# Optimization experiments

Measured on AMD Instinct MI355X. Metric: run time of the kernel, lower is better.

## Reference

```python
import jax, jax.numpy as jnp
import numpy as np
import math

N, E, D = 50000, 800000, 128


def _linear_params(key, d_in, d_out):
    kw, kb = jax.random.split(key)
    s = 1.0 / math.sqrt(d_in)
    W = jax.random.uniform(kw, (d_out, d_in), minval=-s, maxval=s, dtype=jnp.float32)
    b = jax.random.uniform(kb, (d_out,), minval=-s, maxval=s, dtype=jnp.float32)
    return W, b


def setup_inputs() -> dict:
    key = jax.random.key(0)
    ks = jax.random.split(key, 10)
    inp = {
        "x": jax.random.normal(ks[0], (N, D), dtype=jnp.float32),
        "edge_index": jax.random.randint(ks[1], (2, E), 0, N, dtype=jnp.int32),
    }
    # BPPGraphEncoder: two attention layers, each with q/k/v linears (D->D)
    names = ["q1", "k1", "v1", "q2", "k2", "v2"]
    for i, nm in enumerate(names):
        W, b = _linear_params(ks[2 + i], D, D)
        inp[f"W{nm}"], inp[f"b{nm}"] = W, b
    # SecondaryStructureEncoder: two linears (D->D)
    inp["Ws1"], inp["bs1"] = _linear_params(ks[8], D, D)
    inp["Ws2"], inp["bs2"] = _linear_params(ks[9], D, D)
    return inp


def _attention_layer(x, row, col, Wq, bq, Wk, bk, Wv, bv):
    Q = x @ Wq.T + bq          # [N, D]
    K = x @ Wk.T + bk
    V = x @ Wv.T + bv
    # per-edge score, softmax over ALL edges (faithful to F.softmax(scores, dim=0))
    scores = jnp.sum(Q[row] * K[col], axis=-1) / math.sqrt(Q.shape[-1])  # [E]
    alpha = jax.nn.softmax(scores)                                       # [E]
    msg = alpha[:, None] * V[col]                                        # [E, D]
    return jax.ops.segment_sum(msg, row, num_segments=x.shape[0])        # [N, D]


def _ss_layer(x, row, col, W, b, deg):
    agg = jax.ops.segment_sum(x[col], row, num_segments=x.shape[0])
    return jax.nn.relu((agg / deg) @ W.T + b)


def reference(x, edge_index, Wq1, bq1, Wk1, bk1, Wv1, bv1,
              Wq2, bq2, Wk2, bk2, Wv2, bv2, Ws1, bs1, Ws2, bs2):
    row, col = edge_index[0], edge_index[1]
    # BPPGraphEncoder.forward
    h = jax.nn.elu(_attention_layer(x, row, col, Wq1, bq1, Wk1, bk1, Wv1, bv1))
    bpp_out = _attention_layer(h, row, col, Wq2, bq2, Wk2, bk2, Wv2, bv2)
    # SecondaryStructureEncoder.forward (degree-normalized message passing)
    deg = jax.ops.segment_sum(jnp.ones((row.shape[0],), jnp.float32), row,
                              num_segments=x.shape[0])
    deg = jnp.clip(deg, 1.0, None)[:, None]                              # [N, 1]
    s = _ss_layer(x, row, col, Ws1, bs1, deg)
    ss_out = _ss_layer(s, row, col, Ws2, bs2, deg)
    return jnp.concatenate([bpp_out, ss_out], axis=-1)                   # [N, 2D]
```

## Files before the change

### kernel.cpp

```cpp
#include <hip/hip_runtime.h>
#include <math.h>

#define FD 128

typedef __attribute__((ext_vector_type(8))) _Float16 half8v;
typedef __attribute__((ext_vector_type(4))) _Float16 half4v;
typedef __attribute__((ext_vector_type(4))) float float4v;
typedef __attribute__((ext_vector_type(2))) float floatx2;

static __device__ __forceinline__ void dec8(unsigned int lo, unsigned int hi, float* f){
  floatx2 a = __builtin_amdgcn_cvt_pk_f32_fp8(lo, false);
  floatx2 b = __builtin_amdgcn_cvt_pk_f32_fp8(lo, true);
  floatx2 c = __builtin_amdgcn_cvt_pk_f32_fp8(hi, false);
  floatx2 d = __builtin_amdgcn_cvt_pk_f32_fp8(hi, true);
  f[0]=a[0]; f[1]=a[1]; f[2]=b[0]; f[3]=b[1];
  f[4]=c[0]; f[5]=c[1]; f[6]=d[0]; f[7]=d[1];
}

__global__ void k_cvt_x(const float4* __restrict__ in, half4v* __restrict__ out, int n4){
  int i = blockIdx.x * 256 + threadIdx.x, st = gridDim.x * 256;
  for (; i < n4; i += st){
    float4 v = in[i];
    half4v o;
    o[0] = (_Float16)v.x; o[1] = (_Float16)v.y; o[2] = (_Float16)v.z; o[3] = (_Float16)v.w;
    out[i] = o;
  }
}

__global__ __launch_bounds__(256) void k_cvt_w(
    const float* __restrict__ w0, const float* __restrict__ w1, const float* __restrict__ w2,
    const float* __restrict__ w3, const float* __restrict__ w4, const float* __restrict__ w5,
    const float* __restrict__ w6, const float* __restrict__ w7, _Float16* __restrict__ dst){
  int i = blockIdx.x * 256 + threadIdx.x;
  if (i >= FD * FD) return;
  dst[0*FD*FD + i] = (_Float16)w0[i];
  dst[1*FD*FD + i] = (_Float16)w1[i];
  dst[2*FD*FD + i] = (_Float16)w2[i];
  dst[3*FD*FD + i] = (_Float16)w3[i];
  dst[4*FD*FD + i] = (_Float16)w4[i];
  dst[5*FD*FD + i] = (_Float16)w5[i];
  dst[6*FD*FD + i] = (_Float16)w6[i];
  dst[7*FD*FD + i] = (_Float16)w7[i];
}

__global__ void k_count_deg(const int* __restrict__ row, int E, int* __restrict__ deg){
  int i = blockIdx.x * blockDim.x + threadIdx.x;
  int stride = gridDim.x * blockDim.x;
  for (; i < E; i += stride) atomicAdd(&deg[row[i]], 1);
}

__global__ __launch_bounds__(256) void k_scan_blk(const int* __restrict__ in, int n,
    int* __restrict__ out, int* __restrict__ blksum){
  __shared__ int sm[256];
  const int tid = threadIdx.x;
  const int base = blockIdx.x * 1024;
  const int idx = base + tid * 4;
  int v0=0,v1=0,v2=0,v3=0;
  if (idx + 3 < n){ int4 t = *(const int4*)(in + idx); v0=t.x; v1=t.y; v2=t.z; v3=t.w; }
  else {
    if (idx   < n) v0 = in[idx];
    if (idx+1 < n) v1 = in[idx+1];
    if (idx+2 < n) v2 = in[idx+2];
    if (idx+3 < n) v3 = in[idx+3];
  }
  int s = v0+v1+v2+v3;
  sm[tid] = s; __syncthreads();
  for (int off = 1; off < 256; off <<= 1){
    int t = (tid >= off) ? sm[tid-off] : 0;
    __syncthreads();
    sm[tid] += t;
    __syncthreads();
  }
  int excl = sm[tid] - s;
  if (tid == 255) blksum[blockIdx.x] = sm[255];
  if (idx   < n) out[idx]   = excl;
  if (idx+1 < n) out[idx+1] = excl + v0;
  if (idx+2 < n) out[idx+2] = excl + v0 + v1;
  if (idx+3 < n) out[idx+3] = excl + v0 + v1 + v2;
}

__global__ __launch_bounds__(256) void k_scan_part(const int* __restrict__ blksum, int nblk,
    int* __restrict__ blkoff){
  __shared__ int sm[256];
  const int tid = threadIdx.x;
  int v = (tid < nblk) ? blksum[tid] : 0;
  sm[tid] = v; __syncthreads();
  for (int off = 1; off < 256; off <<= 1){
    int t = (tid >= off) ? sm[tid-off] : 0;
    __syncthreads();
    sm[tid] += t;
    __syncthreads();
  }
  if (tid < nblk) blkoff[tid] = sm[tid] - v;
}

__global__ __launch_bounds__(256) void k_scan_add(int* __restrict__ out, int n,
    const int* __restrict__ blkoff, int E){
  int i = blockIdx.x * 256 + threadIdx.x;
  if (i < n) out[i] += blkoff[i >> 10];
  if (i == 0) out[n] = E;
}

__global__ void k_fill_csr(const int* __restrict__ row, const int* __restrict__ col, int E,
                           const int* __restrict__ rowstart, int* __restrict__ cursor,
                           int* __restrict__ csrcol){
  int i = blockIdx.x * blockDim.x + threadIdx.x;
  int stride = gridDim.x * blockDim.x;
  for (; i < E; i += stride){
    int r = row[i];
    int pos = rowstart[r] + atomicAdd(&cursor[r], 1);
    csrcol[pos] = col[i];
  }
}

template<int NOUT, int ACT, int OMODE>
__global__ __launch_bounds__(256) void k_gemm_lds(const _Float16* __restrict__ X, int ldx,
    const _Float16* __restrict__ W,
    const float* __restrict__ b0, void* __restrict__ Y0,
    const float* __restrict__ b1, void* __restrict__ Y1,
    const float* __restrict__ b2, void* __restrict__ Y2,
    int ldy, int nrows)
{
  __shared__ _Float16 sW[FD * FD];
  const int tid  = threadIdx.x;
  const int wid  = tid >> 6;
  const int lane = tid & 63;
  const int l4 = lane & 15;
  const int kg = lane >> 4;
  const int r0 = blockIdx.x * 64 + wid * 16;

  int rA = r0 + l4; if (rA > nrows - 1) rA = nrows - 1;
  half8v xf[4];
  #pragma unroll
  for (int ks = 0; ks < 4; ks++)
    xf[ks] = *(const half8v*)(X + (size_t)rA * ldx + ks*32 + kg*8);

  for (int o = 0; o < NOUT; o++){
    if (o) __syncthreads();
    const _Float16* Wo = W + (size_t)o * FD * FD;
    #pragma unroll
    for (int j = 0; j < 8; j++){
      const int b = j*4096 + tid*16;
      const int row = b >> 8, cb = b & 255;
      half8v v = *(const half8v*)((const char*)Wo + b);
      *(half8v*)((char*)sW + ((row*256 + (cb ^ ((row & 7) << 4))))) = v;
    }
    __syncthreads();

    float4v acc[8];
    #pragma unroll
    for (int t = 0; t < 8; t++)
      #pragma unroll
      for (int i = 0; i < 4; i++) acc[t][i] = 0.f;

    #pragma unroll
    for (int t = 0; t < 8; t++){
      const int row = t*16 + l4;
      const int sw = (row & 7) << 4;
      #pragma unroll
      for (int ks = 0; ks < 4; ks++){
        half8v wf = *(const half8v*)((const char*)sW + (row*256 + ((ks*64 + kg*16) ^ sw)));
        acc[t] = __builtin_amdgcn_mfma_f32_16x16x32_f16(wf, xf[ks], acc[t], 0, 0, 0);
      }
    }

    const float* bo = (o == 0) ? b0 : (o == 1) ? b1 : b2;
    void* Yo = (o == 0) ? Y0 : (o == 1) ? Y1 : Y2;
    const int r = r0 + l4;
    if (r < nrows){
      #pragma unroll
      for (int t = 0; t < 8; t++){
        const int c = t*16 + kg*4;
        const float4 bb = *(const float4*)(bo + c);
        float v0 = acc[t][0] + bb.x, v1 = acc[t][1] + bb.y;
        float v2 = acc[t][2] + bb.z, v3 = acc[t][3] + bb.w;
        if (ACT){ v0=fmaxf(v0,0.f); v1=fmaxf(v1,0.f); v2=fmaxf(v2,0.f); v3=fmaxf(v3,0.f); }
        if (OMODE == 1 && o == 0){
          *(float4*)((float*)Yo + (size_t)r * ldy + c) = make_float4(v0, v1, v2, v3);
        } else if (OMODE == 2 && o > 0){
          unsigned int w01 = (unsigned int)__builtin_amdgcn_cvt_pk_fp8_f32(v0, v1, 0, false);
          unsigned int w   = (unsigned int)__builtin_amdgcn_cvt_pk_fp8_f32(v2, v3, (int)w01, true);
          *(unsigned int*)((unsigned char*)Yo + (size_t)r * FD + c) = w;
        } else {
          half4v hv;
          hv[0]=(_Float16)v0; hv[1]=(_Float16)v1; hv[2]=(_Float16)v2; hv[3]=(_Float16)v3;
          *(half4v*)((_Float16*)Yo + (size_t)r * ldy + c) = hv;
        }
      }
    }
  }
}

#define SC 0.08838834764831845f

#define RED16(d) \
  d += __shfl_xor(d, 1); d += __shfl_xor(d, 2); d += __shfl_xor(d, 4); d += __shfl_xor(d, 8);

__global__ __launch_bounds__(256) void k_passA(const _Float16* __restrict__ Qh,
    const unsigned char* __restrict__ K8, const _Float16* __restrict__ Xh,
    const int* __restrict__ rowstart, const int* __restrict__ csrcol,
    float* __restrict__ scores, _Float16* __restrict__ SMh, int ldsm, int nnodes)
{
  const int tid = threadIdx.x;
  const int n = blockIdx.x * 16 + (tid >> 4);
  if (n >= nnodes) return;
  const int l4 = tid & 15;
  const half8v qv = *(const half8v*)(Qh + (size_t)n * FD + 8*l4);
  float qf[8];
  #pragma unroll
  for (int i = 0; i < 8; i++) qf[i] = (float)qv[i];
  float sx[8];
  #pragma unroll
  for (int i = 0; i < 8; i++) sx[i] = 0.f;
  const int p0 = rowstart[n], p1 = rowstart[n+1];
  const int last = p1 - 1;
  for (int p = p0; p < p1; p += 4){
    int cc[4]; float mk[4];
    #pragma unroll
    for (int j = 0; j < 4; j++){
      const int idx = p + j;
      cc[j] = csrcol[idx < p1 ? idx : last];
      mk[j] = idx < p1 ? 1.f : 0.f;
    }
    uint2 ku[4]; half8v xv[4];
    #pragma unroll
    for (int j = 0; j < 4; j++){
      ku[j] = *(const uint2*)(K8 + (size_t)cc[j]*FD + 8*l4);
      xv[j] = *(const half8v*)(Xh + (size_t)cc[j]*FD + 8*l4);
    }
    float d[4];
    #pragma unroll
    for (int j = 0; j < 4; j++){
      float kf[8];
      dec8(ku[j].x, ku[j].y, kf);
      float t = 0.f;
      #pragma unroll
      for (int i = 0; i < 8; i++) t += qf[i] * kf[i];
      d[j] = t;
      #pragma unroll
      for (int i = 0; i < 8; i++) sx[i] += mk[j] * (float)xv[j][i];
    }
    #pragma unroll
    for (int j = 0; j < 4; j++){ RED16(d[j]) }
    const float sv = (l4==0) ? d[0] : (l4==1) ? d[1] : (l4==2) ? d[2] : d[3];
    if (l4 < 4 && p + l4 < p1) scores[p + l4] = sv * SC;
  }
  int dg = p1 - p0; if (dg < 1) dg = 1;
  const float inv = 1.f / (float)dg;
  half8v o;
  #pragma unroll
  for (int i = 0; i < 8; i++) o[i] = (_Float16)(sx[i]*inv);
  *(half8v*)(SMh + (size_t)n * ldsm + 8*l4) = o;
}

__global__ __launch_bounds__(256) void k_scores2(const _Float16* __restrict__ Qh,
    const unsigned char* __restrict__ K8,
    const int* __restrict__ rowstart, const int* __restrict__ csrcol,
    float* __restrict__ scores, int nnodes)
{
  const int tid = threadIdx.x;
  const int n = blockIdx.x * 16 + (tid >> 4);
  if (n >= nnodes) return;
  const int l4 = tid & 15;
  const int p0 = rowstart[n], p1 = rowstart[n+1];
  if (p0 >= p1) return;
  const half8v qv = *(const half8v*)(Qh + (size_t)n * FD + 8*l4);
  float qf[8];
  #pragma unroll
  for (int i = 0; i < 8; i++) qf[i] = (float)qv[i];
  const int last = p1 - 1;
  for (int p = p0; p < p1; p += 4){
    int cc[4];
    #pragma unroll
    for (int j = 0; j < 4; j++){
      const int idx = p + j;
      cc[j] = csrcol[idx < p1 ? idx : last];
    }
    uint2 ku[4];
    #pragma unroll
    for (int j = 0; j < 4; j++)
      ku[j] = *(const uint2*)(K8 + (size_t)cc[j]*FD + 8*l4);
    float d[4];
    #pragma unroll
    for (int j = 0; j < 4; j++){
      float kf[8];
      dec8(ku[j].x, ku[j].y, kf);
      float t = 0.f;
      #pragma unroll
      for (int i = 0; i < 8; i++) t += qf[i] * kf[i];
      d[j] = t;
    }
    #pragma unroll
    for (int j = 0; j < 4; j++){ RED16(d[j]) }
    const float sv = (l4==0) ? d[0] : (l4==1) ? d[1] : (l4==2) ? d[2] : d[3];
    if (l4 < 4 && p + l4 < p1) scores[p + l4] = sv * SC;
  }
}

__global__ __launch_bounds__(256) void k_passB(const unsigned char* __restrict__ V8,
    const _Float16* __restrict__ Sh,
    const float* __restrict__ sc, const float* __restrict__ Mp, const float* __restrict__ Ip,
    const int* __restrict__ rowstart, const int* __restrict__ csrcol,
    _Float16* __restrict__ Ah, _Float16* __restrict__ Bh, int ldb, int nnodes)
{
  const int tid = threadIdx.x;
  const int n = blockIdx.x * 16 + (tid >> 4);
  if (n >= nnodes) return;
  const int l4 = tid & 15;
  const float M = Mp[0], inv = Ip[0];
  float av[8], sv[8];
  #pragma unroll
  for (int i = 0; i < 8; i++){ av[i] = 0.f; sv[i] = 0.f; }
  const int p0 = rowstart[n], p1 = rowstart[n+1];
  const int last = p1 - 1;
  for (int p = p0; p < p1; p += 4){
    int cc[4]; float aa[4], mk[4];
    #pragma unroll
    for (int j = 0; j < 4; j++){
      const int idx = p + j;
      const int eff = idx < p1 ? idx : last;
      cc[j] = csrcol[eff];
      aa[j] = sc[eff];
      mk[j] = idx < p1 ? 1.f : 0.f;
    }
    uint2 vu[4]; half8v ss[4];
    #pragma unroll
    for (int j = 0; j < 4; j++){
      vu[j] = *(const uint2*)(V8 + (size_t)cc[j]*FD + 8*l4);
      ss[j] = *(const half8v*)(Sh + (size_t)cc[j]*FD + 8*l4);
    }
    #pragma unroll
    for (int j = 0; j < 4; j++){
      const float a = mk[j] * __expf(aa[j] - M);
      float vf[8];
      dec8(vu[j].x, vu[j].y, vf);
      #pragma unroll
      for (int i = 0; i < 8; i++){
        av[i] += a * vf[i];
        sv[i] += mk[j] * (float)ss[j][i];
      }
    }
  }
  #pragma unroll
  for (int i = 0; i < 8; i++){
    float v = av[i] * inv;
    av[i] = v > 0.f ? v : expm1f(v);
  }
  half8v oa;
  #pragma unroll
  for (int i = 0; i < 8; i++) oa[i] = (_Float16)av[i];
  *(half8v*)(Ah + (size_t)n * FD + 8*l4) = oa;
  int dg = p1 - p0; if (dg < 1) dg = 1;
  const float invd = 1.f / (float)dg;
  half8v ob;
  #pragma unroll
  for (int i = 0; i < 8; i++) ob[i] = (_Float16)(sv[i]*invd);
  *(half8v*)(Bh + (size_t)n * ldb + 8*l4) = ob;
}

__global__ __launch_bounds__(256) void k_message2(const unsigned char* __restrict__ V8,
    const float* __restrict__ sc, const float* __restrict__ Mp, const float* __restrict__ Ip,
    const int* __restrict__ rowstart, const int* __restrict__ csrcol,
    float* __restrict__ out, int ldo, int nnodes)
{
  const int tid = threadIdx.x;
  const int n = blockIdx.x * 16 + (tid >> 4);
  if (n >= nnodes) return;
  const int l4 = tid & 15;
  const float M = Mp[0], inv = Ip[0];
  float av[8];
  #pragma unroll
  for (int i = 0; i < 8; i++) av[i] = 0.f;
  const int p0 = rowstart[n], p1 = rowstart[n+1];
  const int last = p1 - 1;
  for (int p = p0; p < p1; p += 4){
    int cc[4]; float aa[4], mk[4];
    #pragma unroll
    for (int j = 0; j < 4; j++){
      const int idx = p + j;
      const int eff = idx < p1 ? idx : last;
      cc[j] = csrcol[eff];
      aa[j] = sc[eff];
      mk[j] = idx < p1 ? 1.f : 0.f;
    }
    uint2 vu[4];
    #pragma unroll
    for (int j = 0; j < 4; j++)
      vu[j] = *(const uint2*)(V8 + (size_t)cc[j]*FD + 8*l4);
    #pragma unroll
    for (int j = 0; j < 4; j++){
      const float a = mk[j] * __expf(aa[j] - M);
      float vf[8];
      dec8(vu[j].x, vu[j].y, vf);
      #pragma unroll
      for (int i = 0; i < 8; i++) av[i] += a * vf[i];
    }
  }
  float* op = out + (size_t)n * ldo + 8*l4;
  *(float4*)(op    ) = make_float4(av[0]*inv, av[1]*inv, av[2]*inv, av[3]*inv);
  *(float4*)(op + 4) = make_float4(av[4]*inv, av[5]*inv, av[6]*inv, av[7]*inv);
}

__global__ __launch_bounds__(256) void k_sm_partial(const float* __restrict__ s, int n,
    float* __restrict__ pm, float* __restrict__ ps){
  __shared__ float sm_m[256], sm_s[256];
  const int tid = threadIdx.x;
  float m = -3.402823466e38f, sum = 0.f;
  const int n4 = n >> 2;
  const float4* s4 = (const float4*)s;
  for (int i = blockIdx.x * 256 + tid; i < n4; i += gridDim.x * 256){
    float4 q = s4[i];
    float vv[4] = {q.x, q.y, q.z, q.w};
    #pragma unroll
    for (int j = 0; j < 4; j++){
      float v = vv[j];
      if (v <= m) sum += __expf(v - m);
      else { sum = sum * __expf(m - v) + 1.f; m = v; }
    }
  }
  if (blockIdx.x == 0 && tid < (n - (n4 << 2))){
    float v = s[(n4 << 2) + tid];
    if (v <= m) sum += __expf(v - m);
    else { sum = sum * __expf(m - v) + 1.f; m = v; }
  }
  sm_m[tid] = m; sm_s[tid] = sum; __syncthreads();
  for (int off = 128; off > 0; off >>= 1){
    if (tid < off){
      float m2 = sm_m[tid + off], s2 = sm_s[tid + off];
      float m1 = sm_m[tid], s1 = sm_s[tid];
      float Mx = fmaxf(m1, m2);
      sm_m[tid] = Mx;
      sm_s[tid] = s1 * __expf(m1 - Mx) + s2 * __expf(m2 - Mx);
    }
    __syncthreads();
  }
  if (tid == 0){ pm[blockIdx.x] = sm_m[0]; ps[blockIdx.x] = sm_s[0]; }
}

__global__ __launch_bounds__(256) void k_sm_final(const float* __restrict__ pm, const float* __restrict__ ps,
    int n, float* __restrict__ Mout, float* __restrict__ Iout){
  __shared__ float sm_m[256], sm_s[256];
  const int tid = threadIdx.x;
  float m = -3.402823466e38f, sum = 0.f;
  for (int i = tid; i < n; i += 256){
    float m2 = pm[i], s2 = ps[i];
    float Mx = fmaxf(m, m2);
    sum = sum * __expf(m - Mx) + s2 * __expf(m2 - Mx);
    m = Mx;
  }
  sm_m[tid] = m; sm_s[tid] = sum; __syncthreads();
  for (int off = 128; off > 0; off >>= 1){
    if (tid < off){
      float m2 = sm_m[tid + off], s2 = sm_s[tid + off];
      float m1 = sm_m[tid], s1 = sm_s[tid];
      float Mx = fmaxf(m1, m2);
      sm_m[tid] = Mx;
      sm_s[tid] = s1 * __expf(m1 - Mx) + s2 * __expf(m2 - Mx);
    }
    __syncthreads();
  }
  if (tid == 0){ Mout[0] = sm_m[0]; Iout[0] = 1.f / sm_s[0]; }
}

extern "C" void kernel_launch(void* const* d_in, const int* in_sizes, int n_in,
                              void* d_out, int out_size, void* d_ws, size_t ws_size,
                              hipStream_t stream)
{
  const float* x   = (const float*)d_in[0];
  const int*   ei  = (const int*)d_in[1];
  const float* Wq1 = (const float*)d_in[2];  const float* bq1 = (const float*)d_in[3];
  const float* Wk1 = (const float*)d_in[4];  const float* bk1 = (const float*)d_in[5];
  const float* Wv1 = (const float*)d_in[6];  const float* bv1 = (const float*)d_in[7];
  const float* Wq2 = (const float*)d_in[8];  const float* bq2 = (const float*)d_in[9];
  const float* Wk2 = (const float*)d_in[10]; const float* bk2 = (const float*)d_in[11];
  const float* Wv2 = (const float*)d_in[12]; const float* bv2 = (const float*)d_in[13];
  const float* Ws1 = (const float*)d_in[14]; const float* bs1 = (const float*)d_in[15];
  const float* Ws2 = (const float*)d_in[16]; const float* bs2 = (const float*)d_in[17];

  const int N = in_sizes[0] / FD;
  const int E = in_sizes[1] / 2;
  const int* row = ei;
  const int* col = ei + E;
  float* out = (float*)d_out;

  char* ws = (char*)d_ws;
  size_t off = 0;
  auto alloc = [&](size_t bytes) -> void* {
    void* p = ws + off;
    off += (bytes + 255) & ~(size_t)255;
    return p;
  };
  int* deg      = (int*)alloc((size_t)N * 4);
  int* rowstart = (int*)alloc((size_t)(N + 1) * 4);
  int* cursor   = (int*)alloc((size_t)N * 4);
  int* csrcol   = (int*)alloc((size_t)E * 4);
  float* scores = (float*)alloc((size_t)E * 4);
  int* blksum   = (int*)alloc(1024);
  int* blkoff   = (int*)alloc(1024);
  float* pm     = (float*)alloc(1024);
  float* ps     = (float*)alloc(1024);
  float* Mv     = (float*)alloc(256);
  float* Iv     = (float*)alloc(256);
  _Float16* Xh = (_Float16*)alloc((size_t)N * FD * 2);
  _Float16* Qh = (_Float16*)alloc((size_t)N * FD * 2);
  unsigned char* K8 = (unsigned char*)alloc((size_t)N * FD);
  unsigned char* V8 = (unsigned char*)alloc((size_t)N * FD);
  _Float16* Ah = (_Float16*)alloc((size_t)N * FD * 2);
  _Float16* Wh = (_Float16*)alloc((size_t)8 * FD * FD * 2);
  _Float16* Sh = Xh;
  _Float16* SMBh = (_Float16*)out;
  (void)ws_size; (void)n_in; (void)out_size;

  hipMemsetAsync(deg, 0, (size_t)N * 4, stream);
  hipMemsetAsync(cursor, 0, (size_t)N * 4, stream);

  k_cvt_x<<<2048, 256, 0, stream>>>((const float4*)x, (half4v*)Xh, N * FD / 4);
  k_cvt_w<<<(FD*FD + 255)/256, 256, 0, stream>>>(Wq1, Wk1, Wv1, Wq2, Wk2, Wv2, Ws1, Ws2, Wh);

  const int eb = 2048;
  const int nblk = (N + 1023) / 1024;
  k_count_deg<<<eb, 256, 0, stream>>>(row, E, deg);
  k_scan_blk<<<nblk, 256, 0, stream>>>(deg, N, rowstart, blksum);
  k_scan_part<<<1, 256, 0, stream>>>(blksum, nblk, blkoff);
  k_scan_add<<<(N + 255)/256, 256, 0, stream>>>(rowstart, N, blkoff, E);
  k_fill_csr<<<eb, 256, 0, stream>>>(row, col, E, rowstart, cursor, csrcol);

  const int gb = (N + 63) / 64;
  const int nb = (N + 15) / 16;
  const int rb = 256;

  k_gemm_lds<3,0,2><<<gb, 256, 0, stream>>>(Xh, FD, Wh + 0*FD*FD,
      bq1, Qh, bk1, K8, bv1, V8, FD, N);

  k_passA<<<nb, 256, 0, stream>>>(Qh, K8, Xh, rowstart, csrcol, scores, SMBh, 512, N);

  k_sm_partial<<<rb, 256, 0, stream>>>(scores, E, pm, ps);
  k_sm_final<<<1, 256, 0, stream>>>(pm, ps, rb, Mv, Iv);

  k_gemm_lds<1,1,0><<<gb, 256, 0, stream>>>(SMBh, 512, Wh + 6*FD*FD,
      bs1, Sh, nullptr, nullptr, nullptr, nullptr, FD, N);

  k_passB<<<nb, 256, 0, stream>>>(V8, Sh, scores, Mv, Iv, rowstart, csrcol, Ah, SMBh, 512, N);

  k_gemm_lds<1,1,1><<<gb, 256, 0, stream>>>(SMBh, 512, Wh + 7*FD*FD,
      bs2, out + FD, nullptr, nullptr, nullptr, nullptr, 2*FD, N);

  k_gemm_lds<3,0,2><<<gb, 256, 0, stream>>>(Ah, FD, Wh + 3*FD*FD,
      bq2, Qh, bk2, K8, bv2, V8, FD, N);
  k_scores2<<<nb, 256, 0, stream>>>(Qh, K8, rowstart, csrcol, scores, N);

  k_sm_partial<<<rb, 256, 0, stream>>>(scores, E, pm, ps);
  k_sm_final<<<1, 256, 0, stream>>>(pm, ps, rb, Mv, Iv);

  k_message2<<<nb, 256, 0, stream>>>(V8, scores, Mv, Iv, rowstart, csrcol, out, 2*FD, N);
}
```

Before: 333.5 us.

## Build CSR via two-level bucket sort with shared-memory atomics

Replaces the global-atomic degree count and CSR fill with a bucketed scheme: edges are histogrammed into buckets of 256 rows, scattered as (row,col) pairs into bucket order, then per-bucket blocks compute degrees and fill CSR columns using LDS atomics. This removes scattered global atomics on a large array, at the cost of extra kernel launches and an extra pass writing and reading an 8-byte pair array. Bucket count is assumed to be at most 256 (N up to 65536), which holds here. The ordering of columns within a row stays nondeterministic, as before.

New measurement: 298.6 us. 1.12x faster.

```diff
diff --git a/kernel.cpp b/kernel.cpp
--- a/kernel.cpp
+++ b/kernel.cpp
@@ -43,10 +43,89 @@
   dst[7*FD*FD + i] = (_Float16)w7[i];
 }
 
-__global__ void k_count_deg(const int* __restrict__ row, int E, int* __restrict__ deg){
-  int i = blockIdx.x * blockDim.x + threadIdx.x;
-  int stride = gridDim.x * blockDim.x;
-  for (; i < E; i += stride) atomicAdd(&deg[row[i]], 1);
+
+__global__ __launch_bounds__(256) void k_bhist(const int* __restrict__ row, int E,
+    int* __restrict__ bhist){
+  __shared__ int h[256];
+  h[threadIdx.x] = 0; __syncthreads();
+  for (int i = blockIdx.x*256 + threadIdx.x; i < E; i += gridDim.x*256)
+    atomicAdd(&h[row[i] >> 8], 1);
+  __syncthreads();
+  int v = h[threadIdx.x];
+  if (v) atomicAdd(&bhist[threadIdx.x], v);
+}
+
+__global__ __launch_bounds__(256) void k_bscan(const int* __restrict__ bhist,
+    int* __restrict__ bstart, int* __restrict__ bcursor, int E){
+  __shared__ int sm[256];
+  const int tid = threadIdx.x;
+  int v = bhist[tid];
+  sm[tid] = v; __syncthreads();
+  for (int off = 1; off < 256; off <<= 1){
+    int t = (tid >= off) ? sm[tid-off] : 0;
+    __syncthreads();
+    sm[tid] += t;
+    __syncthreads();
+  }
+  bstart[tid] = sm[tid] - v;
+  if (tid == 255) bstart[256] = E;
+  bcursor[tid] = 0;
+}
+
+__global__ __launch_bounds__(256) void k_bscatter(const int* __restrict__ row,
+    const int* __restrict__ col, int E, const int* __restrict__ bstart,
+    int* __restrict__ bcursor, uint2* __restrict__ pairs){
+  __shared__ int cnt[256];
+  __shared__ int base[256];
+  const int tid = threadIdx.x;
+  const int per = (E + gridDim.x - 1) / gridDim.x;
+  const int lo = blockIdx.x * per;
+  const int hi = min(E, lo + per);
+  cnt[tid] = 0; __syncthreads();
+  for (int i = lo + tid; i < hi; i += 256)
+    atomicAdd(&cnt[row[i] >> 8], 1);
+  __syncthreads();
+  base[tid] = cnt[tid] ? atomicAdd(&bcursor[tid], cnt[tid]) : 0;
+  __syncthreads();
+  cnt[tid] = 0; __syncthreads();
+  for (int i = lo + tid; i < hi; i += 256){
+    const int r = row[i];
+    const int b = r >> 8;
+    const int loc = atomicAdd(&cnt[b], 1);
+    pairs[(size_t)bstart[b] + base[b] + loc] = make_uint2((unsigned)r, (unsigned)col[i]);
+  }
+}
+
+__global__ __launch_bounds__(256) void k_bdeg(const uint2* __restrict__ pairs,
+    const int* __restrict__ bstart, int N, int* __restrict__ deg){
+  __shared__ int cnt[256];
+  const int b = blockIdx.x, tid = threadIdx.x;
+  cnt[tid] = 0; __syncthreads();
+  const int lo = bstart[b], hi = bstart[b+1];
+  for (int i = lo + tid; i < hi; i += 256)
+    atomicAdd(&cnt[pairs[i].x & 255], 1);
+  __syncthreads();
+  const int r = (b << 8) + tid;
+  if (r < N) deg[r] = cnt[tid];
+}
+
+__global__ __launch_bounds__(256) void k_bfill(const uint2* __restrict__ pairs,
+    const int* __restrict__ bstart, const int* __restrict__ rowstart, int N,
+    int* __restrict__ csrcol){
+  __shared__ int base[256];
+  __shared__ int cur[256];
+  const int b = blockIdx.x, tid = threadIdx.x;
+  const int r = (b << 8) + tid;
+  base[tid] = (r < N) ? rowstart[r] : 0;
+  cur[tid] = 0;
+  __syncthreads();
+  const int lo = bstart[b], hi = bstart[b+1];
+  for (int i = lo + tid; i < hi; i += 256){
+    uint2 p = pairs[i];
+    const int rl = p.x & 255;
+    const int loc = atomicAdd(&cur[rl], 1);
+    csrcol[base[rl] + loc] = (int)p.y;
+  }
 }
 
 __global__ __launch_bounds__(256) void k_scan_blk(const int* __restrict__ in, int n,
@@ -99,18 +178,6 @@
   int i = blockIdx.x * 256 + threadIdx.x;
   if (i < n) out[i] += blkoff[i >> 10];
   if (i == 0) out[n] = E;
-}
-
-__global__ void k_fill_csr(const int* __restrict__ row, const int* __restrict__ col, int E,
-                           const int* __restrict__ rowstart, int* __restrict__ cursor,
-                           int* __restrict__ csrcol){
-  int i = blockIdx.x * blockDim.x + threadIdx.x;
-  int stride = gridDim.x * blockDim.x;
-  for (; i < E; i += stride){
-    int r = row[i];
-    int pos = rowstart[r] + atomicAdd(&cursor[r], 1);
-    csrcol[pos] = col[i];
-  }
 }
 
 template<int NOUT, int ACT, int OMODE>
@@ -492,8 +559,11 @@
   };
   int* deg      = (int*)alloc((size_t)N * 4);
   int* rowstart = (int*)alloc((size_t)(N + 1) * 4);
-  int* cursor   = (int*)alloc((size_t)N * 4);
   int* csrcol   = (int*)alloc((size_t)E * 4);
+  uint2* pairs  = (uint2*)alloc((size_t)E * 8);
+  int* bhist    = (int*)alloc(1024);
+  int* bstart   = (int*)alloc(1056);
+  int* bcursor  = (int*)alloc(1024);
   float* scores = (float*)alloc((size_t)E * 4);
   int* blksum   = (int*)alloc(1024);
   int* blkoff   = (int*)alloc(1024);
@@ -511,19 +581,21 @@
   _Float16* SMBh = (_Float16*)out;
   (void)ws_size; (void)n_in; (void)out_size;
 
-  hipMemsetAsync(deg, 0, (size_t)N * 4, stream);
-  hipMemsetAsync(cursor, 0, (size_t)N * 4, stream);
+  hipMemsetAsync(bhist, 0, 1024, stream);
 
   k_cvt_x<<<2048, 256, 0, stream>>>((const float4*)x, (half4v*)Xh, N * FD / 4);
   k_cvt_w<<<(FD*FD + 255)/256, 256, 0, stream>>>(Wq1, Wk1, Wv1, Wq2, Wk2, Wv2, Ws1, Ws2, Wh);
 
-  const int eb = 2048;
+  const int nbuckets = (N + 255) >> 8;
   const int nblk = (N + 1023) / 1024;
-  k_count_deg<<<eb, 256, 0, stream>>>(row, E, deg);
+  k_bhist<<<1024, 256, 0, stream>>>(row, E, bhist);
+  k_bscan<<<1, 256, 0, stream>>>(bhist, bstart, bcursor, E);
+  k_bscatter<<<256, 256, 0, stream>>>(row, col, E, bstart, bcursor, pairs);
+  k_bdeg<<<nbuckets, 256, 0, stream>>>(pairs, bstart, N, deg);
   k_scan_blk<<<nblk, 256, 0, stream>>>(deg, N, rowstart, blksum);
   k_scan_part<<<1, 256, 0, stream>>>(blksum, nblk, blkoff);
   k_scan_add<<<(N + 255)/256, 256, 0, stream>>>(rowstart, N, blkoff, E);
-  k_fill_csr<<<eb, 256, 0, stream>>>(row, col, E, rowstart, cursor, csrcol);
+  k_bfill<<<nbuckets, 256, 0, stream>>>(pairs, bstart, rowstart, N, csrcol);
 
   const int gb = (N + 63) / 64;
   const int nb = (N + 15) / 16;
```
